# Kernel tuning notes

Hardware: AMD Instinct MI355X
Metric: run time of the kernel (lower is better)

Reference implementation:

```python
import jax, jax.numpy as jnp
import numpy as np

S = 16384   # num src nodes
D = 16384   # num dst nodes
FS = 128    # src feature len
FD = 128    # dst feature len
R = 50.0    # dist threshold (m)
L = 2005.0  # box side so avg degree ~ 32
LN_EPS = 1e-5


def setup_inputs() -> dict:
    rng = np.random.default_rng(0)
    src_pos_np = rng.uniform(0.0, L, (S, 2)).astype(np.float32)
    dst_pos_np = rng.uniform(0.0, L, (D, 2)).astype(np.float32)
    # radius-graph edge construction (data-dependent, done once outside jit)
    es, ed = [], []
    CH = 2048
    for i in range(0, S, CH):
        d = np.linalg.norm(src_pos_np[i:i + CH, None, :] - dst_pos_np[None, :, :], axis=-1)
        si, di = np.nonzero(d <= R)
        es.append((si + i).astype(np.int32))
        ed.append(di.astype(np.int32))
    edge_src_idx = jnp.asarray(np.concatenate(es))
    edge_dst_idx = jnp.asarray(np.concatenate(ed))

    key = jax.random.key(0)
    ks = jax.random.split(key, 12)
    w = lambda k, shape: (jax.random.normal(k, shape, jnp.float32) * 0.02)
    return {
        'src_node_features': jax.random.normal(ks[0], (S, FS), jnp.float32),
        'src_node_pos': jnp.asarray(src_pos_np),
        'dst_node_features': jax.random.normal(ks[1], (D, FD), jnp.float32),
        'dst_node_pos': jnp.asarray(dst_pos_np),
        'src_w': w(ks[2], (FS, FS)), 'src_b': jnp.zeros((FS,), jnp.float32),
        'dst_w': w(ks[3], (FD, FD)), 'dst_b': jnp.zeros((FD,), jnp.float32),
        'dist_w': w(ks[4], (2, FD)), 'dist_b': jnp.zeros((FD,), jnp.float32),
        'edge_w1': w(ks[5], (FS + FD + FD, FD)), 'edge_b1': jnp.zeros((FD,), jnp.float32),
        'edge_w2': w(ks[6], (FD, FD)), 'edge_b2': jnp.zeros((FD,), jnp.float32),
        'ln_g': jnp.ones((FD,), jnp.float32), 'ln_b': jnp.zeros((FD,), jnp.float32),
        'out_w': w(ks[7], (FD, FD)), 'out_b': jnp.zeros((FD,), jnp.float32),
        'edge_src_idx': edge_src_idx,
        'edge_dst_idx': edge_dst_idx,
    }


def reference(src_node_features, src_node_pos, dst_node_features, dst_node_pos,
              src_w, src_b, dst_w, dst_b, dist_w, dist_b,
              edge_w1, edge_b1, edge_w2, edge_b2, ln_g, ln_b, out_w, out_b,
              edge_src_idx, edge_dst_idx):
    # node encoders: Linear + ReLU
    src_enc = jax.nn.relu(src_node_features @ src_w + src_b)   # [S, FS]
    dst_enc = jax.nn.relu(dst_node_features @ dst_w + dst_b)   # [D, FD]
    # gather per-edge
    e_src = src_enc[edge_src_idx]                               # [E, FS]
    e_dst = dst_enc[edge_dst_idx]                               # [E, FD]
    e_dpos = src_node_pos[edge_src_idx] - dst_node_pos[edge_dst_idx]  # [E, 2]
    e_dist = jax.nn.relu(e_dpos @ dist_w + dist_b)              # [E, FD]
    # edge MLP: Linear-ReLU-Linear on concat [E, FS+FD+FD]
    e_in = jnp.concatenate([e_src, e_dist, e_dst], axis=-1)
    e_out = jax.nn.relu(e_in @ edge_w1 + edge_b1) @ edge_w2 + edge_b2  # [E, FD]
    # scatter-add to destination nodes
    agg = dst_enc + jax.ops.segment_sum(e_out, edge_dst_idx, num_segments=D)
    # LayerNorm + ReLU + Linear + residual + ReLU
    mu = jnp.mean(agg, axis=-1, keepdims=True)
    var = jnp.mean(jnp.square(agg - mu), axis=-1, keepdims=True)
    ln = (agg - mu) * jax.lax.rsqrt(var + LN_EPS) * ln_g + ln_b
    h = jax.nn.relu(ln) @ out_w + out_b + dst_node_features
    return jax.nn.relu(h)
```

## Files before the change

### kernel.cpp

```cpp
#include <hip/hip_runtime.h>

typedef unsigned short ushort_t;
typedef unsigned int uint_t;
typedef short bhalf8 __attribute__((ext_vector_type(8)));
typedef float f32x4 __attribute__((ext_vector_type(4)));
typedef float f32x2 __attribute__((ext_vector_type(2)));

#define DEG_CAP 96

__device__ __forceinline__ float b2f(ushort_t u) {
    union { uint_t i; float f; } v; v.i = ((uint_t)u) << 16; return v.f;
}
__device__ __forceinline__ float u2f(uint_t u) {
    union { uint_t i; float f; } v; v.i = u; return v.f;
}
__device__ __forceinline__ ushort_t f2b(float f) {
    union { float f; uint_t i; } v; v.f = f;
    uint_t r = v.i + 0x7fffu + ((v.i >> 16) & 1u);
    return (ushort_t)(r >> 16);
}
__device__ __forceinline__ uint_t f2u(float f) {
    union { float f; uint_t i; } v; v.f = f; return v.i;
}
__device__ __forceinline__ uint_t pack_trunc(float lo, float hi) {
    return (f2u(lo) >> 16) | (f2u(hi) & 0xffff0000u);
}
__device__ __forceinline__ uint_t pack_rhu(float lo, float hi) {
    return ((f2u(lo) + 0x8000u) >> 16) | ((f2u(hi) + 0x8000u) & 0xffff0000u);
}
__device__ __forceinline__ uint_t addpack_trunc(uint_t a, uint_t b) {
    f32x2 A, B;
    A.x = u2f(a << 16); A.y = u2f(a & 0xffff0000u);
    B.x = u2f(b << 16); B.y = u2f(b & 0xffff0000u);
    f32x2 C = A + B;
    return pack_trunc(C.x, C.y);
}

__global__ __launch_bounds__(256) void prep_kernel(
    const float* __restrict__ wsrc, const float* __restrict__ wdst,
    const float* __restrict__ w2,   const float* __restrict__ wout,
    const float* __restrict__ w1,
    ushort_t* __restrict__ msrc, ushort_t* __restrict__ mdst,
    ushort_t* __restrict__ m2,   ushort_t* __restrict__ mout,
    ushort_t* __restrict__ m1a,  ushort_t* __restrict__ m1b,
    ushort_t* __restrict__ m1c,
    const int* __restrict__ esi, const int* __restrict__ edi, int E,
    int* __restrict__ deg, int* __restrict__ bucket,
    int2* __restrict__ edge_sd,
    float* __restrict__ hsum, int countB, int zeroB, int Dn)
{
    int b = blockIdx.x, tid = threadIdx.x;
    if (b < 56) {
        const float* ins[7] = { wsrc, wdst, w2, wout, w1, w1 + 16384, w1 + 32768 };
        ushort_t* outs[7]   = { msrc, mdst, m2, mout, m1a, m1b, m1c };
        int mat = b >> 3;
        const float* in = ins[mat];
        ushort_t* out = outs[mat];
        int flat = (b & 7)*256 + tid;
        int nt = flat >> 8, rem = flat & 255;
        int ks = rem >> 6, lane = rem & 63;
        int q = lane >> 4, m = lane & 15;
        #pragma unroll
        for (int j = 0; j < 8; ++j)
            out[flat*8 + j] = f2b(in[(ks*32 + q*8 + j)*128 + nt*16 + m]);
    } else if (b < 56 + countB) {
        int i = (b - 56)*256 + tid;
        if (i < E) {
            int d = edi[i];
            int p = atomicAdd(&deg[d], 1);
            if (p < DEG_CAP) bucket[(size_t)d*DEG_CAP + p] = esi[i];
        }
    } else {
        int zb = b - 56 - countB;
        float4* h4 = (float4*)hsum;
        int total4 = Dn*32;
        for (int i = zb*256 + tid; i < total4; i += zeroB*256)
            h4[i] = make_float4(0.f, 0.f, 0.f, 0.f);
        uint2* e2 = (uint2*)edge_sd;
        for (int i = zb*256 + tid; i < E; i += zeroB*256)
            e2[i] = make_uint2(0u, 0xFFFFFFFFu);
    }
}

__global__ __launch_bounds__(256) void enc2_kernel(
    const float* __restrict__ src_feat, const float* __restrict__ dst_feat,
    const ushort_t* __restrict__ msrc, const ushort_t* __restrict__ mdst,
    const ushort_t* __restrict__ m1a,  const ushort_t* __restrict__ m1c,
    const float* __restrict__ src_b,   const float* __restrict__ dst_b,
    const float* __restrict__ b1,
    ushort_t* __restrict__ Csrc, ushort_t* __restrict__ Cdst,
    ushort_t* __restrict__ dst_enc,
    const int* __restrict__ deg, int* __restrict__ P,
    int Dn, int Sb, int Db)
{
    int tid = threadIdx.x, blk = blockIdx.x;

    if (blk == Sb + Db) {
        __shared__ int sums[256];
        int per = Dn >> 8;
        const int4* d4 = (const int4*)(deg + tid*per);
        int4 v[16]; int s = 0;
        #pragma unroll
        for (int k = 0; k < 16; ++k) {
            v[k] = d4[k];
            v[k].x = min(v[k].x, DEG_CAP); v[k].y = min(v[k].y, DEG_CAP);
            v[k].z = min(v[k].z, DEG_CAP); v[k].w = min(v[k].w, DEG_CAP);
            s += v[k].x + v[k].y + v[k].z + v[k].w;
        }
        sums[tid] = s;
        __syncthreads();
        for (int off = 1; off < 256; off <<= 1) {
            int x = (tid >= off) ? sums[tid - off] : 0;
            __syncthreads();
            sums[tid] += x;
            __syncthreads();
        }
        int run = sums[tid] - s;
        int4* n4 = (int4*)(P + tid*per);
        #pragma unroll
        for (int k = 0; k < 16; ++k) {
            int4 o;
            o.x = run; run += v[k].x;
            o.y = run; run += v[k].y;
            o.z = run; run += v[k].z;
            o.w = run; run += v[k].w;
            n4[k] = o;
        }
        return;
    }

    __shared__ ushort_t A_l[64*136];
    __shared__ ushort_t E_l[64*136];
    __shared__ float b_l[128];
    __shared__ float b2_l[128];

    const float* A; const ushort_t *W1m, *W2m; const float* bias; const float* bias2;
    ushort_t *outC, *outEnc; int rowbase;
    if (blk < Sb) { A = src_feat; W1m = msrc; W2m = m1a; bias = src_b;
                    outC = Csrc; outEnc = nullptr; rowbase = blk*64; bias2 = nullptr; }
    else          { A = dst_feat; W1m = mdst; W2m = m1c; bias = dst_b;
                    outC = Cdst; outEnc = dst_enc; rowbase = (blk - Sb)*64; bias2 = b1; }

    const float4* A4 = (const float4*)A;
    for (int i = tid; i < 2048; i += 256) {
        int r = i >> 5, c = i & 31;
        float4 v = A4[(size_t)(rowbase + r)*32 + c];
        uint2 u;
        u.x = pack_trunc(v.x, v.y);
        u.y = pack_trunc(v.z, v.w);
        *(uint2*)(A_l + r*136 + c*4) = u;
    }
    if (tid < 128) { b_l[tid] = bias[tid]; b2_l[tid] = bias2 ? bias2[tid] : 0.f; }
    __syncthreads();

    int lane = tid & 63, w = tid >> 6, q = lane >> 4, m = lane & 15;
    const bhalf8* Wv1 = (const bhalf8*)W1m;
    f32x4 acc[4][2] = {};
    #pragma unroll
    for (int ks = 0; ks < 4; ++ks) {
        bhalf8 bf0 = Wv1[((2*w)*4 + ks)*64 + lane];
        bhalf8 bf1 = Wv1[((2*w+1)*4 + ks)*64 + lane];
        #pragma unroll
        for (int mt = 0; mt < 4; ++mt) {
            bhalf8 a = *(const bhalf8*)(A_l + (mt*16 + m)*136 + ks*32 + q*8);
            acc[mt][0] = __builtin_amdgcn_mfma_f32_16x16x32_bf16(a, bf0, acc[mt][0], 0, 0, 0);
            acc[mt][1] = __builtin_amdgcn_mfma_f32_16x16x32_bf16(a, bf1, acc[mt][1], 0, 0, 0);
        }
    }
    #pragma unroll
    for (int mt = 0; mt < 4; ++mt)
    #pragma unroll
    for (int nt = 0; nt < 2; ++nt)
    #pragma unroll
    for (int reg = 0; reg < 4; ++reg) {
        int col = w*32 + nt*16 + m;
        int row = mt*16 + q*4 + reg;
        E_l[row*136 + col] = f2b(fmaxf(acc[mt][nt][reg] + b_l[col], 0.f));
    }
    __syncthreads();

    if (outEnc) {
        for (int i = tid; i < 1024; i += 256) {
            int r = i >> 4, c = i & 15;
            ((uint4*)outEnc)[(size_t)(rowbase + r)*16 + c] = *(const uint4*)(E_l + r*136 + c*8);
        }
    }

    const bhalf8* Wv2 = (const bhalf8*)W2m;
    f32x4 acc2[4][2] = {};
    #pragma unroll
    for (int ks = 0; ks < 4; ++ks) {
        bhalf8 bf0 = Wv2[((2*w)*4 + ks)*64 + lane];
        bhalf8 bf1 = Wv2[((2*w+1)*4 + ks)*64 + lane];
        #pragma unroll
        for (int mt = 0; mt < 4; ++mt) {
            bhalf8 a = *(const bhalf8*)(E_l + (mt*16 + m)*136 + ks*32 + q*8);
            acc2[mt][0] = __builtin_amdgcn_mfma_f32_16x16x32_bf16(a, bf0, acc2[mt][0], 0, 0, 0);
            acc2[mt][1] = __builtin_amdgcn_mfma_f32_16x16x32_bf16(a, bf1, acc2[mt][1], 0, 0, 0);
        }
    }
    #pragma unroll
    for (int mt = 0; mt < 4; ++mt)
    #pragma unroll
    for (int nt = 0; nt < 2; ++nt)
    #pragma unroll
    for (int reg = 0; reg < 4; ++reg) {
        int col = w*32 + nt*16 + m;
        int row = mt*16 + q*4 + reg;
        A_l[row*136 + col] = f2b(acc2[mt][nt][reg] + b2_l[col]);
    }
    __syncthreads();
    for (int i = tid; i < 1024; i += 256) {
        int r = i >> 4, c = i & 15;
        ((uint4*)outC)[(size_t)(rowbase + r)*16 + c] = *(const uint4*)(A_l + r*136 + c*8);
    }
}

__global__ __launch_bounds__(256) void csr_kernel(
    const int* __restrict__ P, const int* __restrict__ deg,
    const int* __restrict__ bucket, int2* __restrict__ edge_sd, int Dn)
{
    int t = blockIdx.x*256 + threadIdx.x;
    int d = t >> 2, pl = t & 3;
    if (d >= Dn) return;
    int st = P[d];
    int n = min(deg[d], DEG_CAP);
    const int* bk = bucket + (size_t)d*DEG_CAP;
    for (int p = pl; p < n; p += 4)
        edge_sd[st + p] = make_int2(bk[p], d);
}

__global__ __launch_bounds__(512, 8) void edge_kernel(
    const ushort_t* __restrict__ Csrc, const ushort_t* __restrict__ Cdst,
    const float* __restrict__ src_pos, const float* __restrict__ dst_pos,
    const int2* __restrict__ edge_sd, int E,
    const ushort_t* __restrict__ w1bm,
    const float* __restrict__ dist_w, const float* __restrict__ dist_b,
    float* __restrict__ hsum)
{
    __shared__ char pool[18432];
    __shared__ char poolG[17408];
    __shared__ int s_l[64], d_l[64], segd[64], segid_l[64];
    __shared__ float2 dxy_l[64];
    __shared__ float dw0_l[128], dw1_l[128], db_l[128];
    __shared__ int nseg_s;

    ushort_t* X    = (ushort_t*)pool;
    ushort_t* Hb   = (ushort_t*)pool;
    ushort_t* G    = (ushort_t*)poolG;
    ushort_t* Smat = (ushort_t*)poolG;

    int tid = threadIdx.x, blk = blockIdx.x;

    if (tid < 128) {
        dw0_l[tid] = dist_w[tid];
        dw1_l[tid] = dist_w[128 + tid];
        db_l[tid]  = dist_b[tid];
    }

    if (tid < 64) {
        int g = blk*64 + tid;
        int s = 0, d = -1;
        float dx = 0.f, dy = 0.f;
        if (g < E) {
            int2 sd = edge_sd[g];
            if (sd.y >= 0) {
                s = sd.x; d = sd.y;
                float2 sp = ((const float2*)src_pos)[s];
                float2 dp = ((const float2*)dst_pos)[d];
                dx = sp.x - dp.x; dy = sp.y - dp.y;
            }
        }
        s_l[tid] = s; d_l[tid] = d;
        dxy_l[tid] = make_float2(dx, dy);
        int dprev = __shfl_up(d, 1);
        bool st = (tid == 0) || (d != dprev);
        unsigned long long smask = __ballot(st);
        int segreg = (int)__popcll(smask << (63 - tid)) - 1;
        segid_l[tid] = segreg;
        if (st) segd[segreg] = (d >= 0) ? d*128 : -1;
        if (tid == 0) nseg_s = (int)__popcll(smask);
    }
    __syncthreads();

    const uint4* cs4 = (const uint4*)Csrc;
    const uint4* cd4 = (const uint4*)Cdst;
    #pragma unroll
    for (int k = 0; k < 2; ++k) {
        int i = tid + k*512;
        int r = i >> 4, c = i & 15;
        uint4 a = cs4[(size_t)s_l[r]*16 + c];
        uint4 b = cd4[(size_t)max(d_l[r], 0)*16 + c];
        uint4 u;
        u.x = addpack_trunc(a.x, b.x);
        u.y = addpack_trunc(a.y, b.y);
        u.z = addpack_trunc(a.z, b.z);
        u.w = addpack_trunc(a.w, b.w);
        *(uint4*)(G + r*136 + c*8) = u;
    }

    {
        int j2 = (tid & 63)*2;
        int r0 = tid >> 6;
        float w00 = dw0_l[j2], w01 = dw0_l[j2+1];
        float w10 = dw1_l[j2], w11 = dw1_l[j2+1];
        float bb0 = db_l[j2],  bb1 = db_l[j2+1];
        #pragma unroll
        for (int k = 0; k < 8; ++k) {
            int r = r0 + k*8;
            float2 dd = dxy_l[r];
            float v0 = fmaxf(fmaf(dd.x, w00, fmaf(dd.y, w10, bb0)), 0.f);
            float v1 = fmaxf(fmaf(dd.x, w01, fmaf(dd.y, w11, bb1)), 0.f);
            *(uint_t*)(X + r*136 + j2) = pack_trunc(v0, v1);
        }
    }
    __syncthreads();

    int lane = tid & 63, w = tid >> 6, q = lane >> 4, m = lane & 15;
    f32x4 acc[4] = {};
    const bhalf8* Wv = (const bhalf8*)w1bm;
    #pragma unroll
    for (int ks = 0; ks < 4; ++ks) {
        bhalf8 bf = Wv[(w*4 + ks)*64 + lane];
        #pragma unroll
        for (int mt = 0; mt < 4; ++mt) {
            bhalf8 a = *(const bhalf8*)(X + (mt*16 + m)*136 + ks*32 + q*8);
            acc[mt] = __builtin_amdgcn_mfma_f32_16x16x32_bf16(a, bf, acc[mt], 0, 0, 0);
        }
    }
    __syncthreads();

    int col = w*16 + m;
    #pragma unroll
    for (int mt = 0; mt < 4; ++mt) {
        int row0 = mt*16 + q*4;
        const ushort_t* gp = G + row0*136 + col;
        float v0 = fmaxf(acc[mt][0] + b2f(gp[0]),   0.f);
        float v1 = fmaxf(acc[mt][1] + b2f(gp[136]), 0.f);
        float v2 = fmaxf(acc[mt][2] + b2f(gp[272]), 0.f);
        float v3 = fmaxf(acc[mt][3] + b2f(gp[408]), 0.f);
        uint2 u;
        u.x = pack_rhu(v0, v1);
        u.y = pack_rhu(v2, v3);
        *(uint2*)(Hb + col*72 + row0) = u;
    }
    __syncthreads();

    int ns = nseg_s;
    int zr = (ns + 15) & ~15;
    for (int i = tid; i < zr*32; i += 512) {
        int seg = i >> 5, r2 = (i & 31)*2;
        uint_t v = (segid_l[r2]   == seg ? 0x3f80u     : 0u)
                 | (segid_l[r2+1] == seg ? 0x3f800000u : 0u);
        *(uint_t*)(Smat + seg*72 + r2) = v;
    }
    __syncthreads();

    const ushort_t* hrow = Hb + col*72 + q*8;
    bhalf8 hb0 = *(const bhalf8*)(hrow);
    bhalf8 hb1 = *(const bhalf8*)(hrow + 32);
    for (int sb = 0; sb*16 < ns; ++sb) {
        const ushort_t* srow = Smat + (sb*16 + m)*72 + q*8;
        bhalf8 a0 = *(const bhalf8*)(srow);
        bhalf8 a1 = *(const bhalf8*)(srow + 32);
        f32x4 o = {};
        o = __builtin_amdgcn_mfma_f32_16x16x32_bf16(a0, hb0, o, 0, 0, 0);
        o = __builtin_amdgcn_mfma_f32_16x16x32_bf16(a1, hb1, o, 0, 0, 0);
        #pragma unroll
        for (int reg = 0; reg < 4; ++reg) {
            int seg = sb*16 + q*4 + reg;
            if (seg < ns) {
                int ofs = segd[seg];
                if (ofs >= 0) atomicAdd(&hsum[(size_t)ofs + col], o[reg]);
            }
        }
    }
}

__global__ __launch_bounds__(256) void aggfinal16_kernel(
    const float* __restrict__ hsum, const ushort_t* __restrict__ w2m,
    const float* __restrict__ b2, const int* __restrict__ deg,
    const ushort_t* __restrict__ dst_enc, const float* __restrict__ ln_g,
    const float* __restrict__ ln_b, const ushort_t* __restrict__ moutm,
    const float* __restrict__ out_b, const float* __restrict__ dst_feat,
    float* __restrict__ out)
{
    __shared__ ushort_t A_l[16*136];
    __shared__ ushort_t E2[16*136];
    __shared__ float ps[64], ps2[64];
    __shared__ float muv[16], invv[16];
    __shared__ float pb2[128], pg[128], plb[128], pob[128];
    __shared__ int dgl[16];

    int tid = threadIdx.x, blk = blockIdx.x;
    int lane = tid & 63, w = tid >> 6, q = lane >> 4, m = lane & 15;

    if (tid < 128) { pb2[tid] = b2[tid]; pg[tid] = ln_g[tid];
                     plb[tid] = ln_b[tid]; pob[tid] = out_b[tid]; }
    if (tid < 16) dgl[tid] = deg[blk*16 + tid];
    {
        int r = tid >> 4, c = tid & 15;
        const float4* hv4 = (const float4*)hsum;
        size_t base = (size_t)(blk*16 + r)*32 + c*2;
        float4 p0 = hv4[base], p1 = hv4[base + 1];
        uint4 u;
        u.x = pack_trunc(p0.x, p0.y);
        u.y = pack_trunc(p0.z, p0.w);
        u.z = pack_trunc(p1.x, p1.y);
        u.w = pack_trunc(p1.z, p1.w);
        *(uint4*)(A_l + r*136 + c*8) = u;
        *(uint4*)(E2 + r*136 + c*8) = ((const uint4*)dst_enc)[(size_t)(blk*16 + r)*16 + c];
    }
    __syncthreads();

    const bhalf8* Wv2 = (const bhalf8*)w2m;
    f32x4 acc[2] = {};
    #pragma unroll
    for (int ks = 0; ks < 4; ++ks) {
        bhalf8 bf0 = Wv2[((2*w)*4 + ks)*64 + lane];
        bhalf8 bf1 = Wv2[((2*w+1)*4 + ks)*64 + lane];
        bhalf8 a = *(const bhalf8*)(A_l + m*136 + ks*32 + q*8);
        acc[0] = __builtin_amdgcn_mfma_f32_16x16x32_bf16(a, bf0, acc[0], 0, 0, 0);
        acc[1] = __builtin_amdgcn_mfma_f32_16x16x32_bf16(a, bf1, acc[1], 0, 0, 0);
    }
    float y[2][4];
    #pragma unroll
    for (int nt = 0; nt < 2; ++nt)
    #pragma unroll
    for (int reg = 0; reg < 4; ++reg) {
        int col = w*32 + nt*16 + m;
        int rowl = q*4 + reg;
        y[nt][reg] = acc[nt][reg] + (float)dgl[rowl]*pb2[col] + b2f(E2[rowl*136 + col]);
    }
    float s[4], s2[4];
    #pragma unroll
    for (int reg = 0; reg < 4; ++reg) {
        s[reg]  = y[0][reg] + y[1][reg];
        s2[reg] = y[0][reg]*y[0][reg] + y[1][reg]*y[1][reg];
    }
    #pragma unroll
    for (int o = 1; o < 16; o <<= 1) {
        #pragma unroll
        for (int reg = 0; reg < 4; ++reg) {
            s[reg]  += __shfl_xor(s[reg],  o);
            s2[reg] += __shfl_xor(s2[reg], o);
        }
    }
    if (m == 0) {
        #pragma unroll
        for (int reg = 0; reg < 4; ++reg) {
            ps[(q*4 + reg)*4 + w]  = s[reg];
            ps2[(q*4 + reg)*4 + w] = s2[reg];
        }
    }
    __syncthreads();
    if (tid < 16) {
        float su = ps[tid*4] + ps[tid*4+1] + ps[tid*4+2] + ps[tid*4+3];
        float sq = ps2[tid*4] + ps2[tid*4+1] + ps2[tid*4+2] + ps2[tid*4+3];
        float mu = su / 128.f;
        float var = sq / 128.f - mu*mu;
        muv[tid] = mu;
        invv[tid] = 1.0f / sqrtf(var + 1e-5f);
    }
    __syncthreads();
    #pragma unroll
    for (int nt = 0; nt < 2; ++nt)
    #pragma unroll
    for (int reg = 0; reg < 4; ++reg) {
        int col = w*32 + nt*16 + m;
        int rowl = q*4 + reg;
        float v = (y[nt][reg] - muv[rowl])*invv[rowl]*pg[col] + plb[col];
        A_l[rowl*136 + col] = f2b(fmaxf(v, 0.f));
    }
    __syncthreads();

    const bhalf8* Wo = (const bhalf8*)moutm;
    f32x4 acc2[2] = {};
    #pragma unroll
    for (int ks = 0; ks < 4; ++ks) {
        bhalf8 bf0 = Wo[((2*w)*4 + ks)*64 + lane];
        bhalf8 bf1 = Wo[((2*w+1)*4 + ks)*64 + lane];
        bhalf8 a = *(const bhalf8*)(A_l + m*136 + ks*32 + q*8);
        acc2[0] = __builtin_amdgcn_mfma_f32_16x16x32_bf16(a, bf0, acc2[0], 0, 0, 0);
        acc2[1] = __builtin_amdgcn_mfma_f32_16x16x32_bf16(a, bf1, acc2[1], 0, 0, 0);
    }
    #pragma unroll
    for (int nt = 0; nt < 2; ++nt)
    #pragma unroll
    for (int reg = 0; reg < 4; ++reg) {
        int col = w*32 + nt*16 + m;
        size_t grow = (size_t)blk*16 + q*4 + reg;
        float v = acc2[nt][reg] + pob[col] + dst_feat[grow*128 + col];
        out[grow*128 + col] = fmaxf(v, 0.f);
    }
}

extern "C" void kernel_launch(void* const* d_in, const int* in_sizes, int n_in,
                              void* d_out, int out_size, void* d_ws, size_t ws_size,
                              hipStream_t stream)
{
    const float* src_feat = (const float*)d_in[0];
    const float* src_pos  = (const float*)d_in[1];
    const float* dst_feat = (const float*)d_in[2];
    const float* dst_pos  = (const float*)d_in[3];
    const float* src_w    = (const float*)d_in[4];
    const float* src_b    = (const float*)d_in[5];
    const float* dst_w    = (const float*)d_in[6];
    const float* dst_b    = (const float*)d_in[7];
    const float* dist_w   = (const float*)d_in[8];
    const float* dist_b   = (const float*)d_in[9];
    const float* w1       = (const float*)d_in[10];
    const float* b1       = (const float*)d_in[11];
    const float* w2       = (const float*)d_in[12];
    const float* b2       = (const float*)d_in[13];
    const float* ln_g     = (const float*)d_in[14];
    const float* ln_b     = (const float*)d_in[15];
    const float* out_w    = (const float*)d_in[16];
    const float* out_b    = (const float*)d_in[17];
    const int* esi        = (const int*)d_in[18];
    const int* edi        = (const int*)d_in[19];
    int E = in_sizes[18];
    int S = in_sizes[0] / 128;
    int D = in_sizes[2] / 128;
    int nTiles = (E + 63) / 64;

    char* ws = (char*)d_ws;
    size_t off = 0;
    auto alloc = [&](size_t bytes) { char* p = ws + off; off += (bytes + 511) & ~(size_t)511; return p; };
    ushort_t* Csrc    = (ushort_t*)alloc((size_t)S*128*2);
    ushort_t* Cdst    = (ushort_t*)alloc((size_t)D*128*2);
    ushort_t* dst_enc = (ushort_t*)alloc((size_t)D*128*2);
    float*    hsum    = (float*)   alloc((size_t)D*128*4);
    ushort_t* t_src   = (ushort_t*)alloc(128*128*2);
    ushort_t* t_dst   = (ushort_t*)alloc(128*128*2);
    ushort_t* t_w2    = (ushort_t*)alloc(128*128*2);
    ushort_t* t_out   = (ushort_t*)alloc(128*128*2);
    ushort_t* t_1a    = (ushort_t*)alloc(128*128*2);
    ushort_t* t_1b    = (ushort_t*)alloc(128*128*2);
    ushort_t* t_1c    = (ushort_t*)alloc(128*128*2);
    int*      deg     = (int*)     alloc((size_t)D*4);
    int*      P       = (int*)     alloc((size_t)D*4);
    int*      bucket  = (int*)     alloc((size_t)D*DEG_CAP*4);
    int2*     edge_sd = (int2*)    alloc((size_t)E*8);

    hipMemsetAsync(deg, 0, (size_t)D*4, stream);

    int countB = (E + 255)/256;
    int zeroB = 256;
    prep_kernel<<<56 + countB + zeroB, 256, 0, stream>>>(
        src_w, dst_w, w2, out_w, w1,
        t_src, t_dst, t_w2, t_out, t_1a, t_1b, t_1c,
        esi, edi, E, deg, bucket, edge_sd, hsum, countB, zeroB, D);

    int Sb = S/64, Db = D/64;
    enc2_kernel<<<Sb + Db + 1, 256, 0, stream>>>(
        src_feat, dst_feat, t_src, t_dst, t_1a, t_1c, src_b, dst_b, b1,
        Csrc, Cdst, dst_enc, deg, P, D, Sb, Db);

    csr_kernel<<<(D*4 + 255)/256, 256, 0, stream>>>(P, deg, bucket, edge_sd, D);

    edge_kernel<<<nTiles, 512, 0, stream>>>(
        Csrc, Cdst, src_pos, dst_pos, edge_sd, E,
        t_1b, dist_w, dist_b, hsum);

    aggfinal16_kernel<<<D/16, 256, 0, stream>>>(
        hsum, t_w2, b2, deg, dst_enc, ln_g, ln_b,
        t_out, out_b, dst_feat, (float*)d_out);
}
```

Before: 200.2 us.

## Prefetch edge gathers early and build segment selector matrix in registers

```diff
diff --git a/kernel.cpp b/kernel.cpp
--- a/kernel.cpp
+++ b/kernel.cpp
@@ -46,7 +46,7 @@
     ushort_t* __restrict__ m1c,
     const int* __restrict__ esi, const int* __restrict__ edi, int E,
     int* __restrict__ deg, int* __restrict__ bucket,
-    int2* __restrict__ edge_sd,
+    int2* __restrict__ edge_sd, int Epad,
     float* __restrict__ hsum, int countB, int zeroB, int Dn)
 {
     int b = blockIdx.x, tid = threadIdx.x;
@@ -77,7 +77,7 @@
         for (int i = zb*256 + tid; i < total4; i += zeroB*256)
             h4[i] = make_float4(0.f, 0.f, 0.f, 0.f);
         uint2* e2 = (uint2*)edge_sd;
-        for (int i = zb*256 + tid; i < E; i += zeroB*256)
+        for (int i = zb*256 + tid; i < Epad; i += zeroB*256)
             e2[i] = make_uint2(0u, 0xFFFFFFFFu);
     }
 }
@@ -239,18 +239,27 @@
     float* __restrict__ hsum)
 {
     __shared__ char pool[18432];
-    __shared__ char poolG[17408];
-    __shared__ int s_l[64], d_l[64], segd[64], segid_l[64];
+    __shared__ ushort_t G[64*136];
+    __shared__ int segd[64];
+    __shared__ ushort_t seg16[64];
     __shared__ float2 dxy_l[64];
     __shared__ float dw0_l[128], dw1_l[128], db_l[128];
     __shared__ int nseg_s;
 
-    ushort_t* X    = (ushort_t*)pool;
-    ushort_t* Hb   = (ushort_t*)pool;
-    ushort_t* G    = (ushort_t*)poolG;
-    ushort_t* Smat = (ushort_t*)poolG;
+    ushort_t* X  = (ushort_t*)pool;
+    ushort_t* Hb = (ushort_t*)pool;
 
     int tid = threadIdx.x, blk = blockIdx.x;
+
+    int r0 = tid >> 4, c16 = tid & 15;
+    const uint4* cs4 = (const uint4*)Csrc;
+    const uint4* cd4 = (const uint4*)Cdst;
+    int2 e0 = edge_sd[blk*64 + r0];
+    int2 e1 = edge_sd[blk*64 + r0 + 32];
+    uint4 ga0 = cs4[(size_t)e0.x*16 + c16];
+    uint4 gb0 = cd4[(size_t)max(e0.y, 0)*16 + c16];
+    uint4 ga1 = cs4[(size_t)e1.x*16 + c16];
+    uint4 gb1 = cd4[(size_t)max(e1.y, 0)*16 + c16];
 
     if (tid < 128) {
         dw0_l[tid] = dist_w[tid];
@@ -259,60 +268,53 @@
     }
 
     if (tid < 64) {
-        int g = blk*64 + tid;
-        int s = 0, d = -1;
+        int2 sd = edge_sd[blk*64 + tid];
+        int s = sd.x, d = sd.y;
         float dx = 0.f, dy = 0.f;
-        if (g < E) {
-            int2 sd = edge_sd[g];
-            if (sd.y >= 0) {
-                s = sd.x; d = sd.y;
-                float2 sp = ((const float2*)src_pos)[s];
-                float2 dp = ((const float2*)dst_pos)[d];
-                dx = sp.x - dp.x; dy = sp.y - dp.y;
-            }
-        }
-        s_l[tid] = s; d_l[tid] = d;
+        if (d >= 0) {
+            float2 sp = ((const float2*)src_pos)[s];
+            float2 dp = ((const float2*)dst_pos)[d];
+            dx = sp.x - dp.x; dy = sp.y - dp.y;
+        }
         dxy_l[tid] = make_float2(dx, dy);
         int dprev = __shfl_up(d, 1);
         bool st = (tid == 0) || (d != dprev);
         unsigned long long smask = __ballot(st);
         int segreg = (int)__popcll(smask << (63 - tid)) - 1;
-        segid_l[tid] = segreg;
+        seg16[tid] = (ushort_t)segreg;
         if (st) segd[segreg] = (d >= 0) ? d*128 : -1;
         if (tid == 0) nseg_s = (int)__popcll(smask);
     }
     __syncthreads();
 
-    const uint4* cs4 = (const uint4*)Csrc;
-    const uint4* cd4 = (const uint4*)Cdst;
-    #pragma unroll
-    for (int k = 0; k < 2; ++k) {
-        int i = tid + k*512;
-        int r = i >> 4, c = i & 15;
-        uint4 a = cs4[(size_t)s_l[r]*16 + c];
-        uint4 b = cd4[(size_t)max(d_l[r], 0)*16 + c];
-        uint4 u;
-        u.x = addpack_trunc(a.x, b.x);
-        u.y = addpack_trunc(a.y, b.y);
-        u.z = addpack_trunc(a.z, b.z);
-        u.w = addpack_trunc(a.w, b.w);
-        *(uint4*)(G + r*136 + c*8) = u;
-    }
-
     {
         int j2 = (tid & 63)*2;
-        int r0 = tid >> 6;
+        int rr = tid >> 6;
         float w00 = dw0_l[j2], w01 = dw0_l[j2+1];
         float w10 = dw1_l[j2], w11 = dw1_l[j2+1];
         float bb0 = db_l[j2],  bb1 = db_l[j2+1];
         #pragma unroll
         for (int k = 0; k < 8; ++k) {
-            int r = r0 + k*8;
+            int r = rr + k*8;
             float2 dd = dxy_l[r];
             float v0 = fmaxf(fmaf(dd.x, w00, fmaf(dd.y, w10, bb0)), 0.f);
             float v1 = fmaxf(fmaf(dd.x, w01, fmaf(dd.y, w11, bb1)), 0.f);
             *(uint_t*)(X + r*136 + j2) = pack_trunc(v0, v1);
         }
+    }
+
+    {
+        uint4 u;
+        u.x = addpack_trunc(ga0.x, gb0.x);
+        u.y = addpack_trunc(ga0.y, gb0.y);
+        u.z = addpack_trunc(ga0.z, gb0.z);
+        u.w = addpack_trunc(ga0.w, gb0.w);
+        *(uint4*)(G + r0*136 + c16*8) = u;
+        u.x = addpack_trunc(ga1.x, gb1.x);
+        u.y = addpack_trunc(ga1.y, gb1.y);
+        u.z = addpack_trunc(ga1.z, gb1.z);
+        u.w = addpack_trunc(ga1.w, gb1.w);
+        *(uint4*)(G + (r0 + 32)*136 + c16*8) = u;
     }
     __syncthreads();
 
@@ -344,25 +346,23 @@
         u.y = pack_rhu(v2, v3);
         *(uint2*)(Hb + col*72 + row0) = u;
     }
-    __syncthreads();
+    __builtin_amdgcn_sched_barrier(0);
 
     int ns = nseg_s;
-    int zr = (ns + 15) & ~15;
-    for (int i = tid; i < zr*32; i += 512) {
-        int seg = i >> 5, r2 = (i & 31)*2;
-        uint_t v = (segid_l[r2]   == seg ? 0x3f80u     : 0u)
-                 | (segid_l[r2+1] == seg ? 0x3f800000u : 0u);
-        *(uint_t*)(Smat + seg*72 + r2) = v;
-    }
-    __syncthreads();
-
+    bhalf8 sv0 = *(const bhalf8*)(seg16 + q*8);
+    bhalf8 sv1 = *(const bhalf8*)(seg16 + 32 + q*8);
     const ushort_t* hrow = Hb + col*72 + q*8;
     bhalf8 hb0 = *(const bhalf8*)(hrow);
     bhalf8 hb1 = *(const bhalf8*)(hrow + 32);
+    const short onebf = (short)0x3f80;
     for (int sb = 0; sb*16 < ns; ++sb) {
-        const ushort_t* srow = Smat + (sb*16 + m)*72 + q*8;
-        bhalf8 a0 = *(const bhalf8*)(srow);
-        bhalf8 a1 = *(const bhalf8*)(srow + 32);
+        short target = (short)(sb*16 + m);
+        bhalf8 a0, a1;
+        #pragma unroll
+        for (int j = 0; j < 8; ++j) {
+            a0[j] = (sv0[j] == target) ? onebf : (short)0;
+            a1[j] = (sv1[j] == target) ? onebf : (short)0;
+        }
         f32x4 o = {};
         o = __builtin_amdgcn_mfma_f32_16x16x32_bf16(a0, hb0, o, 0, 0, 0);
         o = __builtin_amdgcn_mfma_f32_16x16x32_bf16(a1, hb1, o, 0, 0, 0);
@@ -523,6 +523,7 @@
     int S = in_sizes[0] / 128;
     int D = in_sizes[2] / 128;
     int nTiles = (E + 63) / 64;
+    int Epad = nTiles*64;
 
     char* ws = (char*)d_ws;
     size_t off = 0;
@@ -541,7 +542,7 @@
     int*      deg     = (int*)     alloc((size_t)D*4);
     int*      P       = (int*)     alloc((size_t)D*4);
     int*      bucket  = (int*)     alloc((size_t)D*DEG_CAP*4);
-    int2*     edge_sd = (int2*)    alloc((size_t)E*8);
+    int2*     edge_sd = (int2*)    alloc((size_t)Epad*8);
 
     hipMemsetAsync(deg, 0, (size_t)D*4, stream);
 
@@ -550,7 +551,7 @@
     prep_kernel<<<56 + countB + zeroB, 256, 0, stream>>>(
         src_w, dst_w, w2, out_w, w1,
         t_src, t_dst, t_w2, t_out, t_1a, t_1b, t_1c,
-        esi, edi, E, deg, bucket, edge_sd, hsum, countB, zeroB, D);
+        esi, edi, E, deg, bucket, edge_sd, Epad, hsum, countB, zeroB, D);
 
     int Sb = S/64, Db = D/64;
     enc2_kernel<<<Sb + Db + 1, 256, 0, stream>>>(
```

Measured after the change: 199.8 us. No clear change (-0.2%).
